# Performance work log

Hardware: AMD Instinct MI355X
Metric: run time of the kernel (lower is better)

## Reference

```python
import jax, jax.numpy as jnp
import numpy as np

# ---- config constants (SmolLM2Config defaults) ----
N_EMBD = 576
N_HEAD = 9
N_KV = 3
HEAD_DIM = N_EMBD // N_HEAD        # 64
DR = 8                              # low-rank RoPE dim per head
GQA = N_HEAD // N_KV                # 9 // 3 = 3
BLOCK = 4096
ROPE_THETA = 100000.0
GROUP = 64                          # quant group size
RESID = 32                          # residual (full-precision) length
KBITS = 2
VBITS = 2
CLIP = 10000.0
B, S = 2, 2064


def _rope_tables():
    # pre_compute_rope with r=4 frequency indexing -> tables of width 2*r = 8 == DR
    pos = np.arange(BLOCK).astype(np.float32)
    thetas = 1.0 / ROPE_THETA ** (np.arange(0, HEAD_DIM, 2).astype(np.float32) / HEAD_DIM)
    pt = np.outer(pos, thetas)                       # [BLOCK, 32]
    pt = np.concatenate([pt, pt], axis=-1)           # [BLOCK, 64]
    cos, sin = np.cos(pt), np.sin(pt)
    r = 4
    idxs = sorted(sum([[2 * int(k * HEAD_DIM / (2 * r)), 2 * int(k * HEAD_DIM / (2 * r)) + 1]
                       for k in range(r)], []))      # [0,1,16,17,32,33,48,49]
    return jnp.asarray(cos[:, idxs]), jnp.asarray(sin[:, idxs])

COS, SIN = _rope_tables()  # each [BLOCK, DR]


def apply_rope(x):
    # x: [b, h, s, DR]; rotate-half RoPE on the DR low-rank dims
    s = x.shape[2]
    half = DR // 2
    x1, x2 = x[..., :half], x[..., half:]
    rotated = jnp.concatenate([-x2, x1], axis=-1)
    return x * COS[:s, :] + rotated * SIN[:s, :]


def _fake_quant(x, mn, mx, bits):
    levels = 2.0 ** bits - 1.0
    scale = (mx - mn) / levels
    scale = jnp.where(scale == 0, 1.0, scale)
    q = jnp.round((x - mn) / scale)
    return q * scale + mn


def quant_key(k):
    # AsymGroupedQuantizerByChannel: per-channel asym 2-bit over groups of GROUP tokens (STE)
    b, h, s, d = k.shape
    kf = jnp.clip(k, -CLIP, CLIP).reshape(b * h * (s // GROUP), GROUP, d)
    mn = kf.min(axis=1, keepdims=True)
    mx = kf.max(axis=1, keepdims=True)
    deq = _fake_quant(kf, mn, mx, KBITS)
    out = kf + jax.lax.stop_gradient(deq - kf)  # straight-through estimator
    return out.reshape(b, h, s, d)


def quant_value(v):
    # AsymGroupedQuantizer: per-token asym 2-bit over channel groups of size GROUP (== head_dim)
    b, h, s, d = v.shape
    vc = jnp.clip(v, -CLIP, CLIP)
    vg = vc.reshape(b, h, s, d // GROUP, GROUP)
    mn = vg.min(axis=-1, keepdims=True)
    mx = vg.max(axis=-1, keepdims=True)
    deq = _fake_quant(vg, mn, mx, VBITS).reshape(b, h, s, d)
    return vc + jax.lax.stop_gradient(deq - vc)


def maybe_quantize_kv(k, v):
    # KIVI: quantize all but the residual window
    s = k.shape[2]
    key_quant_len = (s // RESID) * RESID     # 2048 for S=2064
    value_quant_len = max(0, s - RESID)      # 2032
    k = jnp.concatenate([quant_key(k[:, :, :key_quant_len]), k[:, :, key_quant_len:]], axis=2)
    v = jnp.concatenate([quant_value(v[:, :, :value_quant_len]), v[:, :, value_quant_len:]], axis=2)
    return k, v


def setup_inputs() -> dict:
    key = jax.random.key(0)
    ks = jax.random.split(key, 7)
    std = 0.02
    return {
        "x": jax.random.normal(ks[0], (B, S, N_EMBD), jnp.float32),
        "q_w": jax.random.normal(ks[1], (N_HEAD * (HEAD_DIM - DR), N_EMBD), jnp.float32) * std,
        "k_w": jax.random.normal(ks[2], (N_KV * (HEAD_DIM - DR), N_EMBD), jnp.float32) * std,
        "v_w": jax.random.normal(ks[3], (N_KV * HEAD_DIM, N_EMBD), jnp.float32) * std,
        "qr_w": jax.random.normal(ks[4], (N_HEAD * DR, N_EMBD), jnp.float32) * std,
        "kr_w": jax.random.normal(ks[5], (N_KV * DR, N_EMBD), jnp.float32) * std,
        "o_w": jax.random.normal(ks[6], (N_EMBD, N_EMBD), jnp.float32) * std,
    }


def reference(x, q_w, k_w, v_w, qr_w, kr_w, o_w):
    b, s, _ = x.shape
    # projections (Linear: x @ W^T), split heads, [b, h, s, d]
    q = (x @ q_w.T).reshape(b, s, N_HEAD, HEAD_DIM - DR).transpose(0, 2, 1, 3)
    k = (x @ k_w.T).reshape(b, s, N_KV, HEAD_DIM - DR).transpose(0, 2, 1, 3)
    v = (x @ v_w.T).reshape(b, s, N_KV, HEAD_DIM).transpose(0, 2, 1, 3)
    qr = apply_rope((x @ qr_w.T).reshape(b, s, N_HEAD, DR).transpose(0, 2, 1, 3))
    kr = apply_rope((x @ kr_w.T).reshape(b, s, N_KV, DR).transpose(0, 2, 1, 3))
    q = jnp.concatenate([q, qr], axis=-1)   # [b, 9, s, 64]
    k = jnp.concatenate([k, kr], axis=-1)   # [b, 3, s, 64]
    # KIVI 2-bit fake-quantization of KV (residual window kept full precision)
    k, v = maybe_quantize_kv(k, v)
    # GQA: expand kv heads to query heads
    k = jnp.repeat(k, GQA, axis=1)
    v = jnp.repeat(v, GQA, axis=1)
    # causal attention
    scale = 1.0 / jnp.sqrt(jnp.float32(HEAD_DIM))
    scores = jnp.einsum('bhqd,bhkd->bhqk', q, k) * scale
    mask = jnp.tril(jnp.ones((s, s), bool))
    scores = jnp.where(mask, scores, -jnp.inf)
    attn = jax.nn.softmax(scores, axis=-1)
    out = jnp.einsum('bhqk,bhkd->bhqd', attn, v)
    out = out.transpose(0, 2, 1, 3).reshape(b, s, N_EMBD)
    return out @ o_w.T
```

## Files before the change

kernel.cpp:

```cpp
#include <hip/hip_runtime.h>
#include <math.h>

#define S_LEN 2064
#define S_PAD 2112
#define NB 2
#define NH 9
#define NKV 3
#define HD 64
#define EMB 576
#define NTOK (NB*S_LEN)
#define LSTR 68
#define KSTR 72

#define QSZ (NB*NH*S_LEN*HD)
#define KSZ (NB*NKV*S_LEN*HD)
#define VSZ (NB*NKV*S_LEN*HD)
#define ASZ (NB*S_LEN*EMB)
#define KPK (NB*NKV*S_PAD*HD)

typedef float  f32x4  __attribute__((ext_vector_type(4)));
typedef short  s16x8  __attribute__((ext_vector_type(8)));

static __device__ __forceinline__ ushort f2bf(float x) {
  union { float f; unsigned u; } a; a.f = x;
  unsigned r = a.u + 0x7fffu + ((a.u >> 16) & 1u);
  return (ushort)(r >> 16);
}
static __device__ __forceinline__ float bf2f(ushort h) {
  union { unsigned u; float f; } a; a.u = ((unsigned)h) << 16;
  return a.f;
}

__global__ __launch_bounds__(256)
void proj_kernel(const float* __restrict__ x,
                 const float* __restrict__ qw, const float* __restrict__ kw,
                 const float* __restrict__ vw, const float* __restrict__ qrw,
                 const float* __restrict__ krw,
                 float* __restrict__ Qb, float* __restrict__ Kb,
                 float* __restrict__ Vb) {
  __shared__ __align__(16) ushort Xhi[64*KSTR];
  __shared__ __align__(16) ushort Xlo[64*KSTR];
  __shared__ __align__(16) ushort Whi[64*KSTR];
  __shared__ __align__(16) ushort Wlo[64*KSTR];

  const int tid  = threadIdx.x;
  const int wave = tid >> 6;
  const int lane = tid & 63;
  const int g    = lane >> 4;
  const int c    = lane & 15;

  const int m0 = blockIdx.x * 64;
  const int n0 = blockIdx.y * 64;

  const int srow = tid >> 2;
  const int sseg = (tid & 3) * 16;
  int gm = m0 + srow; if (gm > NTOK-1) gm = NTOK-1;
  const float* xrow = x + (size_t)gm * EMB;
  const int col = n0 + srow;
  const float* wrow;
  if (col < 504)      wrow = qw  + (size_t)col       * EMB;
  else if (col < 672) wrow = kw  + (size_t)(col-504) * EMB;
  else if (col < 864) wrow = vw  + (size_t)(col-672) * EMB;
  else if (col < 936) wrow = qrw + (size_t)(col-864) * EMB;
  else                wrow = krw + (size_t)(col-936) * EMB;

  f32x4 acc[4];
  #pragma unroll
  for (int n=0;n<4;++n) acc[n] = (f32x4){0.f,0.f,0.f,0.f};

  for (int kc0 = 0; kc0 < EMB; kc0 += 64) {
    __syncthreads();
    {
      float xv[16], wv[16];
      #pragma unroll
      for (int i=0;i<4;++i) {
        float4 x4 = *(const float4*)(xrow + kc0 + sseg + 4*i);
        float4 w4 = *(const float4*)(wrow + kc0 + sseg + 4*i);
        xv[4*i+0]=x4.x; xv[4*i+1]=x4.y; xv[4*i+2]=x4.z; xv[4*i+3]=x4.w;
        wv[4*i+0]=w4.x; wv[4*i+1]=w4.y; wv[4*i+2]=w4.z; wv[4*i+3]=w4.w;
      }
      uint xh[8], xl[8], wh[8], wl[8];
      #pragma unroll
      for (int m=0;m<8;++m) {
        ushort h0 = f2bf(xv[2*m]),   h1 = f2bf(xv[2*m+1]);
        ushort l0 = f2bf(xv[2*m]   - bf2f(h0));
        ushort l1 = f2bf(xv[2*m+1] - bf2f(h1));
        xh[m] = (uint)h0 | ((uint)h1 << 16);
        xl[m] = (uint)l0 | ((uint)l1 << 16);
        ushort g0 = f2bf(wv[2*m]),   g1 = f2bf(wv[2*m+1]);
        ushort k0 = f2bf(wv[2*m]   - bf2f(g0));
        ushort k1 = f2bf(wv[2*m+1] - bf2f(g1));
        wh[m] = (uint)g0 | ((uint)g1 << 16);
        wl[m] = (uint)k0 | ((uint)k1 << 16);
      }
      const int lo = srow*KSTR + sseg;
      *(uint4*)&Xhi[lo]     = make_uint4(xh[0],xh[1],xh[2],xh[3]);
      *(uint4*)&Xhi[lo + 8] = make_uint4(xh[4],xh[5],xh[6],xh[7]);
      *(uint4*)&Xlo[lo]     = make_uint4(xl[0],xl[1],xl[2],xl[3]);
      *(uint4*)&Xlo[lo + 8] = make_uint4(xl[4],xl[5],xl[6],xl[7]);
      *(uint4*)&Whi[lo]     = make_uint4(wh[0],wh[1],wh[2],wh[3]);
      *(uint4*)&Whi[lo + 8] = make_uint4(wh[4],wh[5],wh[6],wh[7]);
      *(uint4*)&Wlo[lo]     = make_uint4(wl[0],wl[1],wl[2],wl[3]);
      *(uint4*)&Wlo[lo + 8] = make_uint4(wl[4],wl[5],wl[6],wl[7]);
    }
    __syncthreads();

    #pragma unroll
    for (int kc=0; kc<2; ++kc) {
      const int d = kc*32 + g*8;
      s16x8 x_h = *(const s16x8*)&Xhi[(16*wave + c)*KSTR + d];
      s16x8 x_l = *(const s16x8*)&Xlo[(16*wave + c)*KSTR + d];
      #pragma unroll
      for (int n=0;n<4;++n) {
        s16x8 w_h = *(const s16x8*)&Whi[(16*n + c)*KSTR + d];
        s16x8 w_l = *(const s16x8*)&Wlo[(16*n + c)*KSTR + d];
        acc[n] = __builtin_amdgcn_mfma_f32_16x16x32_bf16(x_h, w_h, acc[n], 0, 0, 0);
        acc[n] = __builtin_amdgcn_mfma_f32_16x16x32_bf16(x_l, w_h, acc[n], 0, 0, 0);
        acc[n] = __builtin_amdgcn_mfma_f32_16x16x32_bf16(x_h, w_l, acc[n], 0, 0, 0);
        acc[n] = __builtin_amdgcn_mfma_f32_16x16x32_bf16(x_l, w_l, acc[n], 0, 0, 0);
      }
    }
  }

  #pragma unroll
  for (int r=0;r<4;++r) {
    const int row = m0 + 16*wave + 4*g + r;
    if (row >= NTOK) continue;
    const int b = row / S_LEN, s = row % S_LEN;
    #pragma unroll
    for (int n=0;n<4;++n) {
      const int cc = n0 + 16*n + c;
      const float v = acc[n][r];
      if (cc < 504) {
        int h = cc / 56, d = cc % 56;
        Qb[(((size_t)(b*NH+h))*S_LEN + s)*HD + d] = v;
      } else if (cc < 672) {
        int h = (cc-504)/56, d = (cc-504)%56;
        Kb[(((size_t)(b*NKV+h))*S_LEN + s)*HD + d] = v;
      } else if (cc < 864) {
        int h = (cc-672)/64, d = (cc-672)%64;
        Vb[(((size_t)(b*NKV+h))*S_LEN + s)*HD + d] = v;
      } else if (cc < 936) {
        int h = (cc-864)/8, d = 56 + (cc-864)%8;
        Qb[(((size_t)(b*NH+h))*S_LEN + s)*HD + d] = v;
      } else {
        int h = (cc-936)/8, d = 56 + (cc-936)%8;
        Kb[(((size_t)(b*NKV+h))*S_LEN + s)*HD + d] = v;
      }
    }
  }
}

__global__ void rope_kernel(float* __restrict__ Qb, float* __restrict__ Kb) {
  const int idx = blockIdx.x * blockDim.x + threadIdx.x;
  const int total = NB*(NH+NKV)*S_LEN;
  if (idx >= total) return;
  const int s  = idx % S_LEN;
  const int bh = idx / S_LEN;
  const int b  = bh / (NH+NKV), hh = bh % (NH+NKV);
  float* base;
  if (hh < NH) base = Qb + (((size_t)(b*NH + hh))*S_LEN + s)*HD + 56;
  else         base = Kb + (((size_t)(b*NKV + (hh-NH)))*S_LEN + s)*HD + 56;

  float4 a = *(const float4*)(base);
  float4 c = *(const float4*)(base + 4);
  float xv[8] = {a.x,a.y,a.z,a.w,c.x,c.y,c.z,c.w};
  const float es[4] = {0.0f, 2.0f/64.0f, 32.0f/64.0f, 34.0f/64.0f};
  const float ps = (float)s;
  float o[8];
  #pragma unroll
  for (int j=0;j<4;++j) {
    float th  = 1.0f / powf(100000.0f, es[j]);
    float ang = ps * th;
    float cs = cosf(ang), sn = sinf(ang);
    o[j]   = xv[j]*cs   - xv[j+4]*sn;
    o[j+4] = xv[j+4]*cs + xv[j]*sn;
  }
  *(float4*)(base)     = make_float4(o[0],o[1],o[2],o[3]);
  *(float4*)(base + 4) = make_float4(o[4],o[5],o[6],o[7]);
}

__global__ void quant_key_kernel(float* __restrict__ Kb) {
  const int wid  = (blockIdx.x * blockDim.x + threadIdx.x) >> 6;
  const int lane = threadIdx.x & 63;
  if (wid >= NB*NKV*32) return;
  const int bkh = wid >> 5, sg = wid & 31;
  float* base = Kb + ((size_t)bkh*S_LEN + sg*64)*HD + lane;
  float vals[64];
  float mn = 1e30f, mx = -1e30f;
  #pragma unroll
  for (int s=0;s<64;++s) {
    float v = fminf(fmaxf(base[s*HD], -10000.0f), 10000.0f);
    vals[s] = v;
    mn = fminf(mn, v); mx = fmaxf(mx, v);
  }
  float scale = (mx - mn) / 3.0f;
  if (scale == 0.0f) scale = 1.0f;
  #pragma unroll
  for (int s=0;s<64;++s) {
    float q = rintf((vals[s] - mn) / scale);
    base[s*HD] = q * scale + mn;
  }
}

__global__ void quant_value_kernel(float* __restrict__ Vb) {
  const int wid  = (blockIdx.x * blockDim.x + threadIdx.x) >> 6;
  const int lane = threadIdx.x & 63;
  const int total = NB*NKV*2032;
  if (wid >= total) return;
  const int bkh = wid / 2032, s = wid % 2032;
  float* p = Vb + ((size_t)bkh*S_LEN + s)*HD + lane;
  float v = fminf(fmaxf(*p, -10000.0f), 10000.0f);
  float mn = v, mx = v;
  #pragma unroll
  for (int m=1;m<64;m<<=1) {
    mn = fminf(mn, __shfl_xor(mn, m));
    mx = fmaxf(mx, __shfl_xor(mx, m));
  }
  float scale = (mx - mn) / 3.0f;
  if (scale == 0.0f) scale = 1.0f;
  float q = rintf((v - mn) / scale);
  *p = q * scale + mn;
}

__global__ __launch_bounds__(256)
void pack_k_kernel(const float* __restrict__ Kb,
                   ushort* __restrict__ KhiG, ushort* __restrict__ KloG) {
  const int idx = blockIdx.x * blockDim.x + threadIdx.x;
  const int total = NB*NKV*S_PAD*8;
  if (idx >= total) return;
  const int bkv = idx / (S_PAD*8);
  const int rem = idx % (S_PAD*8);
  const int s = rem >> 3, d0 = (rem & 7) * 8;
  uint u_h[4], u_l[4];
  if (s < S_LEN) {
    const float* src = Kb + ((size_t)bkv*S_LEN + s)*HD + d0;
    float4 a = *(const float4*)(src);
    float4 b = *(const float4*)(src + 4);
    float v[8] = {a.x,a.y,a.z,a.w,b.x,b.y,b.z,b.w};
    ushort hb[8], lb[8];
    #pragma unroll
    for (int e=0;e<8;++e) {
      hb[e] = f2bf(v[e]);
      lb[e] = f2bf(v[e] - bf2f(hb[e]));
    }
    #pragma unroll
    for (int m=0;m<4;++m) {
      u_h[m] = (uint)hb[2*m] | ((uint)hb[2*m+1] << 16);
      u_l[m] = (uint)lb[2*m] | ((uint)lb[2*m+1] << 16);
    }
  } else {
    #pragma unroll
    for (int m=0;m<4;++m) { u_h[m] = 0; u_l[m] = 0; }
  }
  const size_t off = ((size_t)bkv*S_PAD + s)*HD + d0;
  *(uint4*)(KhiG + off) = make_uint4(u_h[0],u_h[1],u_h[2],u_h[3]);
  *(uint4*)(KloG + off) = make_uint4(u_l[0],u_l[1],u_l[2],u_l[3]);
}

__global__ __launch_bounds__(256)
void pack_v_kernel(const float* __restrict__ Vb,
                   ushort* __restrict__ VhiT) {
  __shared__ float T[64*LSTR];
  const int tid = threadIdx.x;
  const int bkv = blockIdx.x / 33;
  const int kt  = blockIdx.x % 33;
  const int kbase = kt * 64;

  {
    const int key = tid >> 2, c16 = (tid & 3) * 16;
    const int s = kbase + key;
    if (s < S_LEN) {
      const float* src = Vb + ((size_t)bkv*S_LEN + s)*HD + c16;
      #pragma unroll
      for (int i=0;i<4;++i) {
        float4 v = *(const float4*)(src + 4*i);
        *(float4*)(T + key*LSTR + c16 + 4*i) = v;
      }
    } else {
      #pragma unroll
      for (int i=0;i<4;++i)
        *(float4*)(T + key*LSTR + c16 + 4*i) = make_float4(0.f,0.f,0.f,0.f);
    }
  }
  __syncthreads();
  {
    const int d = tid >> 2, seg = tid & 3;
    ushort hb[16];
    #pragma unroll
    for (int kk=0;kk<16;++kk)
      hb[kk] = f2bf(T[(seg*16 + kk)*LSTR + d]);
    uint uh[8];
    #pragma unroll
    for (int m=0;m<8;++m)
      uh[m] = (uint)hb[2*m] | ((uint)hb[2*m+1] << 16);
    const size_t off = ((size_t)bkv*HD + d)*S_PAD + kbase + seg*16;
    *(uint4*)(VhiT + off)     = make_uint4(uh[0],uh[1],uh[2],uh[3]);
    *(uint4*)(VhiT + off + 8) = make_uint4(uh[4],uh[5],uh[6],uh[7]);
  }
}

__global__ __launch_bounds__(256)
void attn_kernel(const float* __restrict__ Q,
                 const ushort* __restrict__ KhiG, const ushort* __restrict__ KloG,
                 const ushort* __restrict__ VhiT,
                 float* __restrict__ A) {
  __shared__ __align__(16) ushort Khi[64*KSTR];
  __shared__ __align__(16) ushort Klo[64*KSTR];
  __shared__ __align__(16) ushort Vhi[64*KSTR];
  __shared__ __align__(16) ushort Phi[64*KSTR];

  const int tid  = threadIdx.x;
  const int wave = tid >> 6;
  const int lane = tid & 63;
  const int g    = lane >> 4;
  const int c    = lane & 15;

  const int qt = (int)gridDim.x - 1 - (int)blockIdx.x;
  const int bh = blockIdx.y;
  const int b = bh / NH, h = bh % NH, kvh = h / (NH/NKV);
  const int bkv = b*NKV + kvh;
  const float* Qg = Q + ((size_t)(b*NH + h)*S_LEN)*HD;
  const ushort* KhiB = KhiG + (size_t)bkv*S_PAD*HD;
  const ushort* KloB = KloG + (size_t)bkv*S_PAD*HD;
  const ushort* VhiB = VhiT + (size_t)bkv*HD*S_PAD;
  const int qbase = qt * 64;

  s16x8 qhi[2], qlo[2];
  {
    int qrow = qbase + 16*wave + c;
    if (qrow > S_LEN-1) qrow = S_LEN-1;
    #pragma unroll
    for (int kc = 0; kc < 2; ++kc) {
      const float* qp = Qg + (size_t)qrow*HD + kc*32 + g*8;
      float4 q0 = *(const float4*)(qp);
      float4 q1 = *(const float4*)(qp + 4);
      float qv[8] = {q0.x,q0.y,q0.z,q0.w,q1.x,q1.y,q1.z,q1.w};
      #pragma unroll
      for (int e=0;e<8;++e) {
        ushort hi = f2bf(qv[e]);
        ushort lo = f2bf(qv[e] - bf2f(hi));
        qhi[kc][e] = (short)hi;
        qlo[kc][e] = (short)lo;
      }
    }
  }

  f32x4 acc_o[4];
  #pragma unroll
  for (int n=0;n<4;++n) acc_o[n] = (f32x4){0.f,0.f,0.f,0.f};
  float m_i[4], l_i[4];
  #pragma unroll
  for (int r=0;r<4;++r) { m_i[r] = -INFINITY; l_i[r] = 0.f; }

  const int srow = tid >> 3;
  const int sseg = (tid & 7) * 8;

  const int nkt = qt + 1;
  for (int kt = 0; kt < nkt; ++kt) {
    const int kbase = kt * 64;
    __syncthreads();

    #pragma unroll
    for (int it=0; it<2; ++it) {
      const int r = srow + 32*it;
      const size_t kg = ((size_t)(kbase + r))*HD + sseg;
      *(uint4*)&Khi[r*KSTR + sseg] = *(const uint4*)(KhiB + kg);
      *(uint4*)&Klo[r*KSTR + sseg] = *(const uint4*)(KloB + kg);
      const size_t vg = (size_t)r*S_PAD + kbase + sseg;
      *(uint4*)&Vhi[r*KSTR + sseg] = *(const uint4*)(VhiB + vg);
    }
    __syncthreads();

    f32x4 sc[4];
    #pragma unroll
    for (int n=0;n<4;++n) sc[n] = (f32x4){0.f,0.f,0.f,0.f};
    #pragma unroll
    for (int kc=0; kc<2; ++kc) {
      #pragma unroll
      for (int n=0;n<4;++n) {
        const int key = 16*n + c;
        const int d   = kc*32 + g*8;
        s16x8 khf = *(const s16x8*)&Khi[key*KSTR + d];
        s16x8 klf = *(const s16x8*)&Klo[key*KSTR + d];
        sc[n] = __builtin_amdgcn_mfma_f32_16x16x32_bf16(qhi[kc], khf, sc[n], 0, 0, 0);
        sc[n] = __builtin_amdgcn_mfma_f32_16x16x32_bf16(qlo[kc], khf, sc[n], 0, 0, 0);
        sc[n] = __builtin_amdgcn_mfma_f32_16x16x32_bf16(qhi[kc], klf, sc[n], 0, 0, 0);
      }
    }

    const bool diag = (kt == qt);
    #pragma unroll
    for (int r=0;r<4;++r) {
      const int grow = qbase + 16*wave + 4*g + r;
      float s[4];
      #pragma unroll
      for (int n=0;n<4;++n) {
        float sv = sc[n][r] * 0.125f;
        if (diag && (kbase + 16*n + c > grow)) sv = -INFINITY;
        s[n] = sv;
      }
      float rm = fmaxf(fmaxf(s[0],s[1]), fmaxf(s[2],s[3]));
      rm = fmaxf(rm, __shfl_xor(rm, 1));
      rm = fmaxf(rm, __shfl_xor(rm, 2));
      rm = fmaxf(rm, __shfl_xor(rm, 4));
      rm = fmaxf(rm, __shfl_xor(rm, 8));
      const float mn = fmaxf(m_i[r], rm);
      const float al = __expf(m_i[r] - mn);
      float sum = 0.f;
      float pv4[4];
      #pragma unroll
      for (int n=0;n<4;++n) {
        float pv = __expf(s[n] - mn);
        pv4[n] = pv;
        sum += pv;
      }
      sum += __shfl_xor(sum, 1);
      sum += __shfl_xor(sum, 2);
      sum += __shfl_xor(sum, 4);
      sum += __shfl_xor(sum, 8);
      l_i[r] = l_i[r]*al + sum;
      m_i[r] = mn;
      #pragma unroll
      for (int n=0;n<4;++n) acc_o[n][r] *= al;
      #pragma unroll
      for (int n=0;n<4;++n)
        Phi[(16*wave + 4*g + r)*KSTR + 16*n + c] = f2bf(pv4[n]);
    }

    #pragma unroll
    for (int kc=0; kc<2; ++kc) {
      const int pd = kc*32 + g*8;
      s16x8 pfh = *(const s16x8*)&Phi[(16*wave + c)*KSTR + pd];
      #pragma unroll
      for (int n=0;n<4;++n) {
        s16x8 vfh = *(const s16x8*)&Vhi[(16*n + c)*KSTR + pd];
        acc_o[n] = __builtin_amdgcn_mfma_f32_16x16x32_bf16(pfh, vfh, acc_o[n], 0, 0, 0);
      }
    }
  }

  #pragma unroll
  for (int r=0;r<4;++r) {
    const int grow = qbase + 16*wave + 4*g + r;
    if (grow < S_LEN) {
      const float inv = 1.0f / l_i[r];
      #pragma unroll
      for (int n=0;n<4;++n)
        A[((size_t)(b*S_LEN + grow))*EMB + h*HD + 16*n + c] = acc_o[n][r] * inv;
    }
  }
}

__global__ __launch_bounds__(256)
void oproj_kernel(const float* __restrict__ A, const float* __restrict__ ow,
                  float* __restrict__ out) {
  __shared__ __align__(16) ushort Ahi[64*KSTR];
  __shared__ __align__(16) ushort Alo[64*KSTR];
  __shared__ __align__(16) ushort Whi[64*KSTR];
  __shared__ __align__(16) ushort Wlo[64*KSTR];

  const int tid  = threadIdx.x;
  const int wave = tid >> 6;
  const int lane = tid & 63;
  const int g    = lane >> 4;
  const int c    = lane & 15;

  const int m0 = blockIdx.x * 64;
  const int n0 = blockIdx.y * 64;

  const int srow = tid >> 2;
  const int sseg = (tid & 3) * 16;
  int am = m0 + srow; if (am > NTOK-1) am = NTOK-1;
  const float* arow = A  + (size_t)am * EMB;
  const float* wrow = ow + (size_t)(n0 + srow) * EMB;

  f32x4 acc[4];
  #pragma unroll
  for (int n=0;n<4;++n) acc[n] = (f32x4){0.f,0.f,0.f,0.f};

  for (int kc0 = 0; kc0 < EMB; kc0 += 64) {
    __syncthreads();
    {
      float av[16], wv[16];
      #pragma unroll
      for (int i=0;i<4;++i) {
        float4 a4 = *(const float4*)(arow + kc0 + sseg + 4*i);
        float4 w4 = *(const float4*)(wrow + kc0 + sseg + 4*i);
        av[4*i+0]=a4.x; av[4*i+1]=a4.y; av[4*i+2]=a4.z; av[4*i+3]=a4.w;
        wv[4*i+0]=w4.x; wv[4*i+1]=w4.y; wv[4*i+2]=w4.z; wv[4*i+3]=w4.w;
      }
      uint ah[8], al[8], wh[8], wl[8];
      #pragma unroll
      for (int m=0;m<8;++m) {
        ushort h0 = f2bf(av[2*m]),   h1 = f2bf(av[2*m+1]);
        ushort l0 = f2bf(av[2*m]   - bf2f(h0));
        ushort l1 = f2bf(av[2*m+1] - bf2f(h1));
        ah[m] = (uint)h0 | ((uint)h1 << 16);
        al[m] = (uint)l0 | ((uint)l1 << 16);
        ushort g0 = f2bf(wv[2*m]),   g1 = f2bf(wv[2*m+1]);
        ushort m0_ = f2bf(wv[2*m]   - bf2f(g0));
        ushort m1_ = f2bf(wv[2*m+1] - bf2f(g1));
        wh[m] = (uint)g0 | ((uint)g1 << 16);
        wl[m] = (uint)m0_ | ((uint)m1_ << 16);
      }
      const int lo = srow*KSTR + sseg;
      *(uint4*)&Ahi[lo]     = make_uint4(ah[0],ah[1],ah[2],ah[3]);
      *(uint4*)&Ahi[lo + 8] = make_uint4(ah[4],ah[5],ah[6],ah[7]);
      *(uint4*)&Alo[lo]     = make_uint4(al[0],al[1],al[2],al[3]);
      *(uint4*)&Alo[lo + 8] = make_uint4(al[4],al[5],al[6],al[7]);
      *(uint4*)&Whi[lo]     = make_uint4(wh[0],wh[1],wh[2],wh[3]);
      *(uint4*)&Whi[lo + 8] = make_uint4(wh[4],wh[5],wh[6],wh[7]);
      *(uint4*)&Wlo[lo]     = make_uint4(wl[0],wl[1],wl[2],wl[3]);
      *(uint4*)&Wlo[lo + 8] = make_uint4(wl[4],wl[5],wl[6],wl[7]);
    }
    __syncthreads();

    #pragma unroll
    for (int kc=0; kc<2; ++kc) {
      const int d = kc*32 + g*8;
      s16x8 a_h = *(const s16x8*)&Ahi[(16*wave + c)*KSTR + d];
      s16x8 a_l = *(const s16x8*)&Alo[(16*wave + c)*KSTR + d];
      #pragma unroll
      for (int n=0;n<4;++n) {
        s16x8 w_h = *(const s16x8*)&Whi[(16*n + c)*KSTR + d];
        s16x8 w_l = *(const s16x8*)&Wlo[(16*n + c)*KSTR + d];
        acc[n] = __builtin_amdgcn_mfma_f32_16x16x32_bf16(a_h, w_h, acc[n], 0, 0, 0);
        acc[n] = __builtin_amdgcn_mfma_f32_16x16x32_bf16(a_l, w_h, acc[n], 0, 0, 0);
        acc[n] = __builtin_amdgcn_mfma_f32_16x16x32_bf16(a_h, w_l, acc[n], 0, 0, 0);
      }
    }
  }

  #pragma unroll
  for (int r=0;r<4;++r) {
    const int m = m0 + 16*wave + 4*g + r;
    if (m < NTOK) {
      #pragma unroll
      for (int n=0;n<4;++n)
        out[(size_t)m*EMB + n0 + 16*n + c] = acc[n][r];
    }
  }
}

extern "C" void kernel_launch(void* const* d_in, const int* in_sizes, int n_in,
                              void* d_out, int out_size, void* d_ws, size_t ws_size,
                              hipStream_t stream) {
  const float* x   = (const float*)d_in[0];
  const float* qw  = (const float*)d_in[1];
  const float* kw  = (const float*)d_in[2];
  const float* vw  = (const float*)d_in[3];
  const float* qrw = (const float*)d_in[4];
  const float* krw = (const float*)d_in[5];
  const float* ow  = (const float*)d_in[6];
  float* out = (float*)d_out;

  float* ws = (float*)d_ws;
  float* Qb = ws;
  float* Kb = Qb + QSZ;
  float* Vb = Kb + KSZ;
  float* Ab = Vb + VSZ;
  ushort* KhiG = (ushort*)(Ab + ASZ);
  ushort* KloG = KhiG + KPK;
  ushort* VhiT = KloG + KPK;

  dim3 g1((NTOK + 63)/64, 960/64);
  proj_kernel<<<g1, 256, 0, stream>>>(x, qw, kw, vw, qrw, krw, Qb, Kb, Vb);

  {
    int total = NB*(NH+NKV)*S_LEN;
    rope_kernel<<<(total+255)/256, 256, 0, stream>>>(Qb, Kb);
  }

  {
    int kwaves = NB*NKV*32;
    quant_key_kernel<<<(kwaves*64+255)/256, 256, 0, stream>>>(Kb);
    int vwaves = NB*NKV*2032;
    quant_value_kernel<<<(vwaves*64+255)/256, 256, 0, stream>>>(Vb);
  }

  {
    int ksegs = NB*NKV*S_PAD*8;
    pack_k_kernel<<<(ksegs+255)/256, 256, 0, stream>>>(Kb, KhiG, KloG);
    pack_v_kernel<<<NB*NKV*33, 256, 0, stream>>>(Vb, VhiT);
  }

  dim3 ga((S_LEN+63)/64, NB*NH);
  attn_kernel<<<ga, 256, 0, stream>>>(Qb, KhiG, KloG, VhiT, Ab);

  dim3 go((NTOK + 63)/64, EMB/64);
  oproj_kernel<<<go, 256, 0, stream>>>(Ab, ow, out);
}
```

Before: 260.4 us.

## Pair causal query tiles per block and double-buffer K/V staging in attention

Each attention block now handles two query tiles, a short one and a long one (p and 32-p). This evens out causal work across blocks and lets both tiles share every K/V tile load. The K/V staging is double-buffered: the next tile is prefetched into registers while the current one is processed, then written to the alternate LDS buffer, which removes one barrier per iteration. The cost is more LDS and more registers (two sets of accumulators and Q fragments), which may lower occupancy.

```diff
diff --git a/kernel.cpp b/kernel.cpp
--- a/kernel.cpp
+++ b/kernel.cpp
@@ -305,9 +305,9 @@
                  const ushort* __restrict__ KhiG, const ushort* __restrict__ KloG,
                  const ushort* __restrict__ VhiT,
                  float* __restrict__ A) {
-  __shared__ __align__(16) ushort Khi[64*KSTR];
-  __shared__ __align__(16) ushort Klo[64*KSTR];
-  __shared__ __align__(16) ushort Vhi[64*KSTR];
+  __shared__ __align__(16) ushort Khi[2][64*KSTR];
+  __shared__ __align__(16) ushort Klo[2][64*KSTR];
+  __shared__ __align__(16) ushort Vhi[2][64*KSTR];
   __shared__ __align__(16) ushort Phi[64*KSTR];
 
   const int tid  = threadIdx.x;
@@ -316,7 +316,9 @@
   const int g    = lane >> 4;
   const int c    = lane & 15;
 
-  const int qt = (int)gridDim.x - 1 - (int)blockIdx.x;
+  const int p   = blockIdx.x;
+  const int qtb = 32 - p;
+  const int qta = (p < 16) ? p : -1;
   const int bh = blockIdx.y;
   const int b = bh / NH, h = bh % NH, kvh = h / (NH/NKV);
   const int bkv = b*NKV + kvh;
@@ -324,10 +326,9 @@
   const ushort* KhiB = KhiG + (size_t)bkv*S_PAD*HD;
   const ushort* KloB = KloG + (size_t)bkv*S_PAD*HD;
   const ushort* VhiB = VhiT + (size_t)bkv*HD*S_PAD;
-  const int qbase = qt * 64;
-
-  s16x8 qhi[2], qlo[2];
-  {
+
+  s16x8 qhiA[2], qloA[2], qhiB2[2], qloB2[2];
+  auto loadQ = [&](int qbase, s16x8* qhi, s16x8* qlo) {
     int qrow = qbase + 16*wave + c;
     if (qrow > S_LEN-1) qrow = S_LEN-1;
     #pragma unroll
@@ -344,34 +345,44 @@
         qlo[kc][e] = (short)lo;
       }
     }
-  }
-
-  f32x4 acc_o[4];
-  #pragma unroll
-  for (int n=0;n<4;++n) acc_o[n] = (f32x4){0.f,0.f,0.f,0.f};
-  float m_i[4], l_i[4];
-  #pragma unroll
-  for (int r=0;r<4;++r) { m_i[r] = -INFINITY; l_i[r] = 0.f; }
+  };
+  loadQ((qta >= 0 ? qta : 0)*64, qhiA, qloA);
+  loadQ(qtb*64, qhiB2, qloB2);
+
+  f32x4 accA[4], accB[4];
+  float mA[4], lA[4], mB[4], lB[4];
+  #pragma unroll
+  for (int n=0;n<4;++n) { accA[n] = (f32x4){0.f,0.f,0.f,0.f}; accB[n] = (f32x4){0.f,0.f,0.f,0.f}; }
+  #pragma unroll
+  for (int r=0;r<4;++r) { mA[r] = -INFINITY; lA[r] = 0.f; mB[r] = -INFINITY; lB[r] = 0.f; }
 
   const int srow = tid >> 3;
   const int sseg = (tid & 7) * 8;
-
-  const int nkt = qt + 1;
-  for (int kt = 0; kt < nkt; ++kt) {
-    const int kbase = kt * 64;
-    __syncthreads();
-
+  uint4 pk_h[2], pk_l[2], pv_h[2];
+  auto stage_load = [&](int kbase) {
     #pragma unroll
     for (int it=0; it<2; ++it) {
       const int r = srow + 32*it;
       const size_t kg = ((size_t)(kbase + r))*HD + sseg;
-      *(uint4*)&Khi[r*KSTR + sseg] = *(const uint4*)(KhiB + kg);
-      *(uint4*)&Klo[r*KSTR + sseg] = *(const uint4*)(KloB + kg);
+      pk_h[it] = *(const uint4*)(KhiB + kg);
+      pk_l[it] = *(const uint4*)(KloB + kg);
       const size_t vg = (size_t)r*S_PAD + kbase + sseg;
-      *(uint4*)&Vhi[r*KSTR + sseg] = *(const uint4*)(VhiB + vg);
-    }
-    __syncthreads();
-
+      pv_h[it] = *(const uint4*)(VhiB + vg);
+    }
+  };
+  auto stage_write = [&](int buf) {
+    #pragma unroll
+    for (int it=0; it<2; ++it) {
+      const int r = srow + 32*it;
+      *(uint4*)&Khi[buf][r*KSTR + sseg] = pk_h[it];
+      *(uint4*)&Klo[buf][r*KSTR + sseg] = pk_l[it];
+      *(uint4*)&Vhi[buf][r*KSTR + sseg] = pv_h[it];
+    }
+  };
+
+  auto process = [&](int buf, int kbase, int qbase, bool diag,
+                     s16x8 (&qhi)[2], s16x8 (&qlo)[2],
+                     f32x4 (&acc)[4], float (&m_i)[4], float (&l_i)[4]) {
     f32x4 sc[4];
     #pragma unroll
     for (int n=0;n<4;++n) sc[n] = (f32x4){0.f,0.f,0.f,0.f};
@@ -381,15 +392,13 @@
       for (int n=0;n<4;++n) {
         const int key = 16*n + c;
         const int d   = kc*32 + g*8;
-        s16x8 khf = *(const s16x8*)&Khi[key*KSTR + d];
-        s16x8 klf = *(const s16x8*)&Klo[key*KSTR + d];
+        s16x8 khf = *(const s16x8*)&Khi[buf][key*KSTR + d];
+        s16x8 klf = *(const s16x8*)&Klo[buf][key*KSTR + d];
         sc[n] = __builtin_amdgcn_mfma_f32_16x16x32_bf16(qhi[kc], khf, sc[n], 0, 0, 0);
         sc[n] = __builtin_amdgcn_mfma_f32_16x16x32_bf16(qlo[kc], khf, sc[n], 0, 0, 0);
         sc[n] = __builtin_amdgcn_mfma_f32_16x16x32_bf16(qhi[kc], klf, sc[n], 0, 0, 0);
       }
     }
-
-    const bool diag = (kt == qt);
     #pragma unroll
     for (int r=0;r<4;++r) {
       const int grow = qbase + 16*wave + 4*g + r;
@@ -422,34 +431,51 @@
       l_i[r] = l_i[r]*al + sum;
       m_i[r] = mn;
       #pragma unroll
-      for (int n=0;n<4;++n) acc_o[n][r] *= al;
+      for (int n=0;n<4;++n) acc[n][r] *= al;
       #pragma unroll
       for (int n=0;n<4;++n)
         Phi[(16*wave + 4*g + r)*KSTR + 16*n + c] = f2bf(pv4[n]);
     }
-
     #pragma unroll
     for (int kc=0; kc<2; ++kc) {
       const int pd = kc*32 + g*8;
       s16x8 pfh = *(const s16x8*)&Phi[(16*wave + c)*KSTR + pd];
       #pragma unroll
       for (int n=0;n<4;++n) {
-        s16x8 vfh = *(const s16x8*)&Vhi[(16*n + c)*KSTR + pd];
-        acc_o[n] = __builtin_amdgcn_mfma_f32_16x16x32_bf16(pfh, vfh, acc_o[n], 0, 0, 0);
-      }
-    }
-  }
-
-  #pragma unroll
-  for (int r=0;r<4;++r) {
-    const int grow = qbase + 16*wave + 4*g + r;
-    if (grow < S_LEN) {
-      const float inv = 1.0f / l_i[r];
-      #pragma unroll
-      for (int n=0;n<4;++n)
-        A[((size_t)(b*S_LEN + grow))*EMB + h*HD + 16*n + c] = acc_o[n][r] * inv;
-    }
-  }
+        s16x8 vfh = *(const s16x8*)&Vhi[buf][(16*n + c)*KSTR + pd];
+        acc[n] = __builtin_amdgcn_mfma_f32_16x16x32_bf16(pfh, vfh, acc[n], 0, 0, 0);
+      }
+    }
+  };
+
+  stage_load(0);
+  stage_write(0);
+  int cur = 0;
+
+  for (int kt = 0; kt <= qtb; ++kt) {
+    __syncthreads();
+    if (kt < qtb) stage_load((kt+1)*64);
+    if (kt <= qta)
+      process(cur, kt*64, qta*64, kt==qta, qhiA, qloA, accA, mA, lA);
+    process(cur, kt*64, qtb*64, kt==qtb, qhiB2, qloB2, accB, mB, lB);
+    if (kt < qtb) stage_write(cur^1);
+    cur ^= 1;
+  }
+
+  auto epi = [&](int qbase, f32x4 (&acc)[4], float (&l_i)[4]) {
+    #pragma unroll
+    for (int r=0;r<4;++r) {
+      const int grow = qbase + 16*wave + 4*g + r;
+      if (grow < S_LEN) {
+        const float inv = 1.0f / l_i[r];
+        #pragma unroll
+        for (int n=0;n<4;++n)
+          A[((size_t)(b*S_LEN + grow))*EMB + h*HD + 16*n + c] = acc[n][r] * inv;
+      }
+    }
+  };
+  if (qta >= 0) epi(qta*64, accA, lA);
+  epi(qtb*64, accB, lB);
 }
 
 __global__ __launch_bounds__(256)
@@ -585,7 +611,7 @@
     pack_v_kernel<<<NB*NKV*33, 256, 0, stream>>>(Vb, VhiT);
   }
 
-  dim3 ga((S_LEN+63)/64, NB*NH);
+  dim3 ga(17, NB*NH);
   attn_kernel<<<ga, 256, 0, stream>>>(Qb, KhiG, KloG, VhiT, Ab);
 
   dim3 go((NTOK + 63)/64, EMB/64);
```

After: 267.9 us. 2.9% more time.

## Split causal attention over KV chunks with partial-softmax reduce kernel

Applied to the files above, without the earlier changes.

Adds a flash-decoding style split of the KV loop in the attention kernel: long query tiles are divided into chunks of 8 KV tiles, each handled by a separate block that writes unnormalized output, max and sum partials to workspace. A new reduce kernel merges the partials with log-sum-exp weighting and writes the normalized output. This targets the load imbalance and limited grid size of causal attention (the last query tiles do 33 iterations while only 594 blocks exist). It costs extra workspace traffic, a second launch, and relies on the workspace being large enough, with a fallback to the unsplit path otherwise.

```diff
diff --git a/kernel.cpp b/kernel.cpp
--- a/kernel.cpp
+++ b/kernel.cpp
@@ -18,6 +18,9 @@
 #define ASZ (NB*S_LEN*EMB)
 #define KPK (NB*NKV*S_PAD*HD)
 
+#define NSLOT_BH 85
+#define NSLOTS (NB*NH*NSLOT_BH)
+
 typedef float  f32x4  __attribute__((ext_vector_type(4)));
 typedef short  s16x8  __attribute__((ext_vector_type(8)));
 
@@ -29,6 +32,10 @@
 static __device__ __forceinline__ float bf2f(ushort h) {
   union { unsigned u; float f; } a; a.u = ((unsigned)h) << 16;
   return a.f;
+}
+static __device__ __forceinline__ int cum8(int qt) {
+  int a = qt >> 3, b = qt & 7;
+  return (a + 1) * (4 * a + b);
 }
 
 __global__ __launch_bounds__(256)
@@ -304,7 +311,9 @@
 void attn_kernel(const float* __restrict__ Q,
                  const ushort* __restrict__ KhiG, const ushort* __restrict__ KloG,
                  const ushort* __restrict__ VhiT,
-                 float* __restrict__ A) {
+                 float* __restrict__ A,
+                 float* __restrict__ Opart, float* __restrict__ Mpart,
+                 float* __restrict__ Lpart, int CK) {
   __shared__ __align__(16) ushort Khi[64*KSTR];
   __shared__ __align__(16) ushort Klo[64*KSTR];
   __shared__ __align__(16) ushort Vhi[64*KSTR];
@@ -316,8 +325,14 @@
   const int g    = lane >> 4;
   const int c    = lane & 15;
 
-  const int qt = (int)gridDim.x - 1 - (int)blockIdx.x;
+  const int qt = 32 - (int)blockIdx.x;
   const int bh = blockIdx.y;
+  const int ch = blockIdx.z;
+  const int nch = (qt + CK) / CK;
+  if (ch >= nch) return;
+  const int kt0 = ch * CK;
+  const int kt1 = min(kt0 + CK, qt + 1);
+
   const int b = bh / NH, h = bh % NH, kvh = h / (NH/NKV);
   const int bkv = b*NKV + kvh;
   const float* Qg = Q + ((size_t)(b*NH + h)*S_LEN)*HD;
@@ -356,8 +371,7 @@
   const int srow = tid >> 3;
   const int sseg = (tid & 7) * 8;
 
-  const int nkt = qt + 1;
-  for (int kt = 0; kt < nkt; ++kt) {
+  for (int kt = kt0; kt < kt1; ++kt) {
     const int kbase = kt * 64;
     __syncthreads();
 
@@ -440,16 +454,83 @@
     }
   }
 
-  #pragma unroll
-  for (int r=0;r<4;++r) {
-    const int grow = qbase + 16*wave + 4*g + r;
-    if (grow < S_LEN) {
-      const float inv = 1.0f / l_i[r];
+  if (nch == 1) {
+    #pragma unroll
+    for (int r=0;r<4;++r) {
+      const int grow = qbase + 16*wave + 4*g + r;
+      if (grow < S_LEN) {
+        const float inv = 1.0f / l_i[r];
+        #pragma unroll
+        for (int n=0;n<4;++n)
+          A[((size_t)(b*S_LEN + grow))*EMB + h*HD + 16*n + c] = acc_o[n][r] * inv;
+      }
+    }
+  } else {
+    const int slot = bh*NSLOT_BH + cum8(qt) + ch;
+    float* Ob = Opart + (size_t)slot * 4096;
+    #pragma unroll
+    for (int r=0;r<4;++r) {
+      const int row = 16*wave + 4*g + r;
       #pragma unroll
       for (int n=0;n<4;++n)
-        A[((size_t)(b*S_LEN + grow))*EMB + h*HD + 16*n + c] = acc_o[n][r] * inv;
-    }
-  }
+        Ob[row*64 + 16*n + c] = acc_o[n][r];
+      if (c == 0) {
+        Mpart[(size_t)slot*64 + row] = m_i[r];
+        Lpart[(size_t)slot*64 + row] = l_i[r];
+      }
+    }
+  }
+}
+
+__global__ __launch_bounds__(256)
+void attn_reduce_kernel(const float* __restrict__ Opart,
+                        const float* __restrict__ Mpart,
+                        const float* __restrict__ Lpart,
+                        float* __restrict__ A) {
+  const int qt = 8 + (int)blockIdx.x;
+  const int bh = blockIdx.y;
+  const int b = bh / NH, h = bh % NH;
+  const int nch = (qt + 8) / 8;
+  const int base = bh*NSLOT_BH + cum8(qt);
+
+  const int tid = threadIdx.x;
+  const int row = tid >> 2;
+  const int seg = (tid & 3) * 16;
+  const int grow = qt*64 + row;
+  if (grow >= S_LEN) return;
+
+  float mv[5], lv[5];
+  float M = -INFINITY;
+  for (int ch=0; ch<nch; ++ch) {
+    mv[ch] = Mpart[(size_t)(base+ch)*64 + row];
+    lv[ch] = Lpart[(size_t)(base+ch)*64 + row];
+    M = fmaxf(M, mv[ch]);
+  }
+  float L = 0.f;
+  float w[5];
+  for (int ch=0; ch<nch; ++ch) {
+    w[ch] = __expf(mv[ch] - M);
+    L += lv[ch] * w[ch];
+  }
+  float o[16];
+  #pragma unroll
+  for (int j=0;j<16;++j) o[j] = 0.f;
+  for (int ch=0; ch<nch; ++ch) {
+    const float* Ob = Opart + (size_t)(base+ch)*4096 + row*64 + seg;
+    const float wc = w[ch];
+    #pragma unroll
+    for (int i=0;i<4;++i) {
+      float4 v = *(const float4*)(Ob + 4*i);
+      o[4*i+0] += wc*v.x; o[4*i+1] += wc*v.y;
+      o[4*i+2] += wc*v.z; o[4*i+3] += wc*v.w;
+    }
+  }
+  const float inv = 1.0f / L;
+  float* dst = A + ((size_t)(b*S_LEN + grow))*EMB + h*HD + seg;
+  #pragma unroll
+  for (int i=0;i<4;++i)
+    *(float4*)(dst + 4*i) = make_float4(o[4*i]*inv, o[4*i+1]*inv,
+                                        o[4*i+2]*inv, o[4*i+3]*inv);
 }
 
 __global__ __launch_bounds__(256)
@@ -563,6 +644,12 @@
   ushort* KhiG = (ushort*)(Ab + ASZ);
   ushort* KloG = KhiG + KPK;
   ushort* VhiT = KloG + KPK;
+  float* Opart = (float*)(VhiT + KPK);
+  float* Mpart = Opart + (size_t)NSLOTS*4096;
+  float* Lpart = Mpart + (size_t)NSLOTS*64;
+
+  const size_t need = (size_t)((char*)(Lpart + (size_t)NSLOTS*64) - (char*)d_ws);
+  const bool splitk = (ws_size >= need);
 
   dim3 g1((NTOK + 63)/64, 960/64);
   proj_kernel<<<g1, 256, 0, stream>>>(x, qw, kw, vw, qrw, krw, Qb, Kb, Vb);
@@ -585,8 +672,17 @@
     pack_v_kernel<<<NB*NKV*33, 256, 0, stream>>>(Vb, VhiT);
   }
 
-  dim3 ga((S_LEN+63)/64, NB*NH);
-  attn_kernel<<<ga, 256, 0, stream>>>(Qb, KhiG, KloG, VhiT, Ab);
+  if (splitk) {
+    dim3 ga(33, NB*NH, 5);
+    attn_kernel<<<ga, 256, 0, stream>>>(Qb, KhiG, KloG, VhiT, Ab,
+                                        Opart, Mpart, Lpart, 8);
+    dim3 gr(25, NB*NH);
+    attn_reduce_kernel<<<gr, 256, 0, stream>>>(Opart, Mpart, Lpart, Ab);
+  } else {
+    dim3 ga(33, NB*NH, 1);
+    attn_kernel<<<ga, 256, 0, stream>>>(Qb, KhiG, KloG, VhiT, Ab,
+                                        Opart, Mpart, Lpart, 33);
+  }
 
   dim3 go((NTOK + 63)/64, EMB/64);
   oproj_kernel<<<go, 256, 0, stream>>>(Ab, ow, out);
```

Result: faster. 220.4 us (-15.4%).
